# Kernel tuning notes

Measured on AMD Instinct MI355X. Metric: run time of the kernel, lower is better.

The kernel has to match this reference:

```python
import jax, jax.numpy as jnp
import numpy as np

S, B, T, A = 512, 64, 768, 512
H1 = (T + T) // 2   # 768
H2 = (T + A) // 2   # 640


def setup_inputs() -> dict:
    key = jax.random.key(0)
    ks = jax.random.split(key, 11)
    sc = 0.02
    return {
        "text": jax.random.normal(ks[0], (B, T), jnp.float32),
        "anp": jax.random.normal(ks[1], (B, A), jnp.float32),
        "text_seq": jax.random.normal(ks[2], (S, B, T), jnp.float32),
        "W11": jax.random.normal(ks[3], (2 * T, H1), jnp.float32) * sc,
        "b11": jax.random.normal(ks[4], (H1,), jnp.float32) * sc,
        "W21": jax.random.normal(ks[5], (H1, 1), jnp.float32) * sc,
        "b21": jax.random.normal(ks[6], (1,), jnp.float32) * sc,
        "W12": jax.random.normal(ks[7], (T + A, H2), jnp.float32) * sc,
        "b12": jax.random.normal(ks[8], (H2,), jnp.float32) * sc,
        "W22": jax.random.normal(ks[9], (H2, 1), jnp.float32) * sc,
        "b22": jax.random.normal(ks[10], (1,), jnp.float32) * sc,
    }


def reference(text, anp, text_seq, W11, b11, W21, b21, W12, b12, W22, b22):
    t = text_seq.shape[-1]
    # cat([text_seq[i], text]) @ W11 == text_seq @ W11[:t] + text @ W11[t:]
    h1 = jnp.tanh(jnp.einsum("sbt,th->sbh", text_seq, W11[:t]) + text @ W11[t:] + b11)
    h2 = jnp.tanh(jnp.einsum("sbt,th->sbh", text_seq, W12[:t]) + anp @ W12[t:] + b12)
    s1 = h1 @ W21 + b21            # (S, B, 1)
    s2 = h2 @ W22 + b22            # (S, B, 1)
    w1 = jax.nn.softmax(s1, axis=0)
    w2 = jax.nn.softmax(s2, axis=0)
    return jnp.mean((w1 + w2) * text_seq * 0.5, axis=0)  # (B, T)
```

## Files before the change

kernel.cpp:

```cpp
#include <hip/hip_runtime.h>
#include <stdint.h>

#define S_DIM 512
#define B_DIM 64
#define T_DIM 768
#define A_DIM 512
#define H1_DIM 768
#define H2_DIM 640
#define N_DIM (H1_DIM + H2_DIM)
#define M_DIM (S_DIM * B_DIM)
#define K_DIM T_DIM
#define NSLOT 22

typedef short s16x8 __attribute__((ext_vector_type(8)));
typedef float f32x4 __attribute__((ext_vector_type(4)));

__device__ __forceinline__ unsigned short f2bf(float f) {
    unsigned u = __float_as_uint(f);
    u += 0x7fffu + ((u >> 16) & 1u);
    return (unsigned short)(u >> 16);
}

#define BIAS_BLKS  (22 * 8)
#define ZOUT_BLKS  12
#define CONVW_BLKS (22 * 12)
#define CONVA_BLKS (M_DIM * K_DIM / 4 / 1024)
#define PREP_BLKS  (BIAS_BLKS + ZOUT_BLKS + CONVW_BLKS + CONVA_BLKS)

__global__ __launch_bounds__(256) void prep_kernel(const float* __restrict__ ts,
                                                   const float* __restrict__ text,
                                                   const float* __restrict__ anp,
                                                   const float* __restrict__ W11,
                                                   const float* __restrict__ b11,
                                                   const float* __restrict__ W12,
                                                   const float* __restrict__ b12,
                                                   unsigned short* __restrict__ Abf,
                                                   unsigned short* __restrict__ Bt,
                                                   float* __restrict__ cbias,
                                                   float* __restrict__ out) {
    const int blk = blockIdx.x;
    __shared__ float lds[64 * 65];
    if (blk < BIAS_BLKS) {
        const int c = blk >> 3;
        const int g = blk & 7;
        const int w = threadIdx.x >> 6;
        const int l = threadIdx.x & 63;
        float acc[8] = {0.f, 0.f, 0.f, 0.f, 0.f, 0.f, 0.f, 0.f};
        int n;
        if (c < 12) {
            n = c * 64 + l;
            const float* wcol = W11 + (size_t)T_DIM * H1_DIM + n;
            const int k0 = w * 192;
            #pragma unroll 4
            for (int k = k0; k < k0 + 192; ++k) {
                float wv = wcol[(size_t)k * H1_DIM];
                #pragma unroll
                for (int i = 0; i < 8; ++i)
                    acc[i] = fmaf(text[(g * 8 + i) * T_DIM + k], wv, acc[i]);
            }
        } else {
            n = H1_DIM + (c - 12) * 64 + l;
            const float* wcol = W12 + (size_t)T_DIM * H2_DIM + (n - H1_DIM);
            const int k0 = w * 128;
            #pragma unroll 4
            for (int k = k0; k < k0 + 128; ++k) {
                float wv = wcol[(size_t)k * H2_DIM];
                #pragma unroll
                for (int i = 0; i < 8; ++i)
                    acc[i] = fmaf(anp[(g * 8 + i) * A_DIM + k], wv, acc[i]);
            }
        }
        #pragma unroll
        for (int i = 0; i < 8; ++i) red_store: lds[w * 512 + i * 64 + l] = acc[i];
        __syncthreads();
        const int i2 = threadIdx.x >> 6;
        const float base = (c < 12) ? b11[n] : b12[n - H1_DIM];
        #pragma unroll
        for (int rep = 0; rep < 2; ++rep) {
            const int i = i2 + rep * 4;
            float s = (lds[i * 64 + l] + lds[512 + i * 64 + l]) +
                      (lds[1024 + i * 64 + l] + lds[1536 + i * 64 + l]);
            cbias[(g * 8 + i) * N_DIM + n] = base + s;
        }
    } else if (blk < BIAS_BLKS + ZOUT_BLKS) {
        const int i0 = (blk - BIAS_BLKS) * 1024 + threadIdx.x;
        float4 z = {0.f, 0.f, 0.f, 0.f};
        float4* o4 = (float4*)out;
        o4[i0] = z; o4[i0 + 256] = z; o4[i0 + 512] = z; o4[i0 + 768] = z;
    } else if (blk < BIAS_BLKS + ZOUT_BLKS + CONVW_BLKS) {
        const int t  = blk - BIAS_BLKS - ZOUT_BLKS;
        const int nt = t / 12, kt = t % 12;
        const int n0 = nt * 64, k0 = kt * 64;
        const int lo = threadIdx.x & 63;
        const int hi = threadIdx.x >> 6;
        const float* Wp;  int ld;
        if (nt < 12) { Wp = W11 + n0;            ld = H1_DIM; }
        else         { Wp = W12 + (n0 - H1_DIM); ld = H2_DIM; }
        #pragma unroll
        for (int r = 0; r < 16; ++r) {
            int kl = hi * 16 + r;
            lds[kl * 65 + lo] = Wp[(size_t)(k0 + kl) * ld + lo];
        }
        __syncthreads();
        #pragma unroll
        for (int r = 0; r < 16; ++r) {
            int nl = hi * 16 + r;
            Bt[(size_t)(n0 + nl) * K_DIM + k0 + lo] = f2bf(lds[lo * 65 + nl]);
        }
    } else {
        int i0 = (blk - BIAS_BLKS - ZOUT_BLKS - CONVW_BLKS) * 1024 + threadIdx.x;
        float4 v0 = ((const float4*)ts)[i0];
        float4 v1 = ((const float4*)ts)[i0 + 256];
        float4 v2 = ((const float4*)ts)[i0 + 512];
        float4 v3 = ((const float4*)ts)[i0 + 768];
        ushort4 o0, o1, o2, o3;
        o0.x = f2bf(v0.x); o0.y = f2bf(v0.y); o0.z = f2bf(v0.z); o0.w = f2bf(v0.w);
        o1.x = f2bf(v1.x); o1.y = f2bf(v1.y); o1.z = f2bf(v1.z); o1.w = f2bf(v1.w);
        o2.x = f2bf(v2.x); o2.y = f2bf(v2.y); o2.z = f2bf(v2.z); o2.w = f2bf(v2.w);
        o3.x = f2bf(v3.x); o3.y = f2bf(v3.y); o3.z = f2bf(v3.z); o3.w = f2bf(v3.w);
        ((ushort4*)Abf)[i0]       = o0;
        ((ushort4*)Abf)[i0 + 256] = o1;
        ((ushort4*)Abf)[i0 + 512] = o2;
        ((ushort4*)Abf)[i0 + 768] = o3;
    }
}

#define BM 128
#define BN 128
#define BK 64

__global__ __launch_bounds__(256, 3) void gemm_score_kernel(
        const unsigned short* __restrict__ A,
        const unsigned short* __restrict__ Bt,
        const float* __restrict__ cbias,
        const float* __restrict__ W21,
        const float* __restrict__ W22,
        float* __restrict__ part) {
    __shared__ __align__(16) unsigned short As[BM * BK];
    __shared__ __align__(16) unsigned short Bs[BN * BK];
    const int tid  = threadIdx.x;
    const int lb   = blockIdx.x;
    const int xcd  = lb & 7;
    const int ib   = lb >> 3;
    const int m0   = ((ib / 11) * 8 + xcd) * BM;
    const int n0   = (ib % 11) * BN;
    const int lane = tid & 63;
    const int wave = tid >> 6;
    const int wm   = wave & 1;
    const int wn   = wave >> 1;
    const int quad = lane >> 4;
    const int col  = lane & 15;
    const int cswz = col & 7;

    f32x4 acc[4][4] = {};

    const int wrow = lane >> 3;
    const int kof  = (((lane & 7) ^ wrow) & 7) * 8;

    for (int k0 = 0; k0 < K_DIM; k0 += BK) {
        #pragma unroll
        for (int p = 0; p < 4; ++p) {
            const int r0 = p * 32 + wave * 8;
            __builtin_amdgcn_global_load_lds(
                (__attribute__((address_space(1))) void*)&A[(size_t)(m0 + r0 + wrow) * K_DIM + k0 + kof],
                (__attribute__((address_space(3))) void*)&As[r0 * BK],
                16, 0, 0);
            __builtin_amdgcn_global_load_lds(
                (__attribute__((address_space(1))) void*)&Bt[(size_t)(n0 + r0 + wrow) * K_DIM + k0 + kof],
                (__attribute__((address_space(3))) void*)&Bs[r0 * BK],
                16, 0, 0);
        }
        __syncthreads();
        #pragma unroll
        for (int kk = 0; kk < BK; kk += 32) {
            s16x8 af[4], bf[4];
            const int ch = ((kk >> 3) + quad) ^ cswz;
            #pragma unroll
            for (int i = 0; i < 4; ++i)
                af[i] = *(const s16x8*)&As[(wm * 64 + i * 16 + col) * BK + ch * 8];
            #pragma unroll
            for (int j = 0; j < 4; ++j)
                bf[j] = *(const s16x8*)&Bs[(wn * 64 + j * 16 + col) * BK + ch * 8];
            #pragma unroll
            for (int i = 0; i < 4; ++i)
                #pragma unroll
                for (int j = 0; j < 4; ++j)
                    acc[i][j] = __builtin_amdgcn_mfma_f32_16x16x32_bf16(af[i], bf[j], acc[i][j], 0, 0, 0);
        }
        __syncthreads();
    }

    const int half = (n0 >= H1_DIM) ? 1 : 0;
    const int jb   = n0 >> 7;
    const float* w2p = half ? (W22 - H1_DIM) : W21;
    int   ncol[4];
    float w2v[4];
    #pragma unroll
    for (int j = 0; j < 4; ++j) {
        ncol[j] = n0 + wn * 64 + j * 16 + col;
        w2v[j]  = w2p[ncol[j]];
    }
    float* pc = part + (jb * 2 + wn) * M_DIM;
    #pragma unroll
    for (int i = 0; i < 4; ++i) {
        #pragma unroll
        for (int r = 0; r < 4; ++r) {
            int row_local = wm * 64 + i * 16 + quad * 4 + r;
            int b = row_local & (B_DIM - 1);
            int s = (m0 + row_local) >> 6;
            float v = 0.f;
            #pragma unroll
            for (int j = 0; j < 4; ++j) {
                float pre = acc[i][j][r] + cbias[b * N_DIM + ncol[j]];
                float ex  = __expf(2.f * pre);
                float th  = 1.f - 2.f * __builtin_amdgcn_rcpf(ex + 1.f);
                v = fmaf(th, w2v[j], v);
            }
            v += __shfl_xor(v, 1);
            v += __shfl_xor(v, 2);
            v += __shfl_xor(v, 4);
            v += __shfl_xor(v, 8);
            if (col == 0) pc[b * S_DIM + s] = v;
        }
    }
}

__global__ __launch_bounds__(512) void softmax_kernel(const float* __restrict__ part,
                                                      float* __restrict__ wsum) {
    const int b = blockIdx.x, s = threadIdx.x;
    __shared__ float redm[16], reds[16];
    float v0 = 0.f, v1 = 0.f;
    #pragma unroll
    for (int sl = 0; sl < 12; ++sl)       v0 += part[sl * M_DIM + b * S_DIM + s];
    #pragma unroll
    for (int sl = 12; sl < NSLOT; ++sl)   v1 += part[sl * M_DIM + b * S_DIM + s];
    float m0 = v0, m1 = v1;
    #pragma unroll
    for (int off = 32; off > 0; off >>= 1) {
        m0 = fmaxf(m0, __shfl_xor(m0, off));
        m1 = fmaxf(m1, __shfl_xor(m1, off));
    }
    const int w = s >> 6;
    if ((s & 63) == 0) { redm[w] = m0; redm[8 + w] = m1; }
    __syncthreads();
    m0 = redm[0]; m1 = redm[8];
    #pragma unroll
    for (int i = 1; i < 8; ++i) { m0 = fmaxf(m0, redm[i]); m1 = fmaxf(m1, redm[8 + i]); }
    float e0 = expf(v0 - m0), e1 = expf(v1 - m1);
    float s0 = e0, s1 = e1;
    #pragma unroll
    for (int off = 32; off > 0; off >>= 1) {
        s0 += __shfl_xor(s0, off);
        s1 += __shfl_xor(s1, off);
    }
    if ((s & 63) == 0) { reds[w] = s0; reds[8 + w] = s1; }
    __syncthreads();
    s0 = reds[0]; s1 = reds[8];
    #pragma unroll
    for (int i = 1; i < 8; ++i) { s0 += reds[i]; s1 += reds[8 + i]; }
    wsum[b * S_DIM + s] = e0 / s0 + e1 / s1;
}

__global__ __launch_bounds__(128) void wmean_kernel(const unsigned short* __restrict__ Abf,
                                                    const float* __restrict__ wsum,
                                                    float* __restrict__ out) {
    const int b  = blockIdx.x;
    const int tp = blockIdx.y * 128 + threadIdx.x;
    const int s0 = blockIdx.z * 128;
    const unsigned short* base = Abf + (size_t)b * T_DIM + tp * 2;
    const float* wp = wsum + b * S_DIM;
    float a0 = 0.f, a1 = 0.f, c0 = 0.f, c1 = 0.f;
    #pragma unroll 4
    for (int s = s0; s < s0 + 128; s += 2) {
        float w0 = wp[s], w1 = wp[s + 1];
        unsigned u0 = *(const unsigned*)(base + (size_t)s * (B_DIM * T_DIM));
        unsigned u1 = *(const unsigned*)(base + (size_t)(s + 1) * (B_DIM * T_DIM));
        a0 = fmaf(w0, __uint_as_float(u0 << 16),          a0);
        a1 = fmaf(w0, __uint_as_float(u0 & 0xffff0000u),  a1);
        c0 = fmaf(w1, __uint_as_float(u1 << 16),          c0);
        c1 = fmaf(w1, __uint_as_float(u1 & 0xffff0000u),  c1);
    }
    atomicAdd(&out[b * T_DIM + tp * 2],     (a0 + c0) * (0.5f / (float)S_DIM));
    atomicAdd(&out[b * T_DIM + tp * 2 + 1], (a1 + c1) * (0.5f / (float)S_DIM));
}

extern "C" void kernel_launch(void* const* d_in, const int* in_sizes, int n_in,
                              void* d_out, int out_size, void* d_ws, size_t ws_size,
                              hipStream_t stream) {
    const float* text = (const float*)d_in[0];
    const float* anp  = (const float*)d_in[1];
    const float* ts   = (const float*)d_in[2];
    const float* W11  = (const float*)d_in[3];
    const float* b11  = (const float*)d_in[4];
    const float* W21  = (const float*)d_in[5];
    const float* W12  = (const float*)d_in[7];
    const float* b12  = (const float*)d_in[8];
    const float* W22  = (const float*)d_in[9];
    float* out = (float*)d_out;

    char* ws = (char*)d_ws;
    unsigned short* Abf = (unsigned short*)ws;
    unsigned short* Bt  = (unsigned short*)(ws + 50331648);
    float* cbias = (float*)(ws + 50331648 + 2162688);
    float* part  = (float*)(ws + 50331648 + 2162688 + 360448);
    float* wsum  = (float*)(ws + 50331648 + 2162688 + 360448 + 2883584);

    prep_kernel<<<PREP_BLKS, 256, 0, stream>>>(
        ts, text, anp, W11, b11, W12, b12, Abf, Bt, cbias, out);
    gemm_score_kernel<<<(M_DIM / BM) * (N_DIM / BN), 256, 0, stream>>>(
        Abf, Bt, cbias, W21, W22, part);
    softmax_kernel<<<B_DIM, 512, 0, stream>>>(part, wsum);
    wmean_kernel<<<dim3(B_DIM, 3, 4), 128, 0, stream>>>(Abf, wsum, out);
}
```

Baseline: 298.3 us.

## Fuse bf16 conversion of activations into GEMM loads and merge softmax with weighted mean

The separate pass that converts text_seq to a bf16 copy is removed. The GEMM now reads fp32 text_seq through registers, packs it to bf16 and writes it to swizzled LDS itself. The softmax and weighted-mean kernels are merged: each block recomputes the softmax for its batch row, then reduces fp32 text_seq over S in LDS. This drops the output zeroing and the atomics. It saves writing and rereading the 50 MB bf16 copy, but the GEMM A-tile load is now synchronous through registers instead of global_load_lds, and the mean pass reads fp32 with the softmax recomputed 12 times per batch row.

```diff
diff --git a/kernel.cpp b/kernel.cpp
--- a/kernel.cpp
+++ b/kernel.cpp
@@ -21,23 +21,22 @@
     return (unsigned short)(u >> 16);
 }
 
+__device__ __forceinline__ unsigned pk2(float a, float b) {
+    return (unsigned)f2bf(a) | ((unsigned)f2bf(b) << 16);
+}
+
 #define BIAS_BLKS  (22 * 8)
-#define ZOUT_BLKS  12
 #define CONVW_BLKS (22 * 12)
-#define CONVA_BLKS (M_DIM * K_DIM / 4 / 1024)
-#define PREP_BLKS  (BIAS_BLKS + ZOUT_BLKS + CONVW_BLKS + CONVA_BLKS)
-
-__global__ __launch_bounds__(256) void prep_kernel(const float* __restrict__ ts,
-                                                   const float* __restrict__ text,
+#define PREP_BLKS  (BIAS_BLKS + CONVW_BLKS)
+
+__global__ __launch_bounds__(256) void prep_kernel(const float* __restrict__ text,
                                                    const float* __restrict__ anp,
                                                    const float* __restrict__ W11,
                                                    const float* __restrict__ b11,
                                                    const float* __restrict__ W12,
                                                    const float* __restrict__ b12,
-                                                   unsigned short* __restrict__ Abf,
                                                    unsigned short* __restrict__ Bt,
-                                                   float* __restrict__ cbias,
-                                                   float* __restrict__ out) {
+                                                   float* __restrict__ cbias) {
     const int blk = blockIdx.x;
     __shared__ float lds[64 * 65];
     if (blk < BIAS_BLKS) {
@@ -71,7 +70,7 @@
             }
         }
         #pragma unroll
-        for (int i = 0; i < 8; ++i) red_store: lds[w * 512 + i * 64 + l] = acc[i];
+        for (int i = 0; i < 8; ++i) lds[w * 512 + i * 64 + l] = acc[i];
         __syncthreads();
         const int i2 = threadIdx.x >> 6;
         const float base = (c < 12) ? b11[n] : b12[n - H1_DIM];
@@ -82,13 +81,8 @@
                       (lds[1024 + i * 64 + l] + lds[1536 + i * 64 + l]);
             cbias[(g * 8 + i) * N_DIM + n] = base + s;
         }
-    } else if (blk < BIAS_BLKS + ZOUT_BLKS) {
-        const int i0 = (blk - BIAS_BLKS) * 1024 + threadIdx.x;
-        float4 z = {0.f, 0.f, 0.f, 0.f};
-        float4* o4 = (float4*)out;
-        o4[i0] = z; o4[i0 + 256] = z; o4[i0 + 512] = z; o4[i0 + 768] = z;
-    } else if (blk < BIAS_BLKS + ZOUT_BLKS + CONVW_BLKS) {
-        const int t  = blk - BIAS_BLKS - ZOUT_BLKS;
+    } else {
+        const int t  = blk - BIAS_BLKS;
         const int nt = t / 12, kt = t % 12;
         const int n0 = nt * 64, k0 = kt * 64;
         const int lo = threadIdx.x & 63;
@@ -107,21 +101,6 @@
             int nl = hi * 16 + r;
             Bt[(size_t)(n0 + nl) * K_DIM + k0 + lo] = f2bf(lds[lo * 65 + nl]);
         }
-    } else {
-        int i0 = (blk - BIAS_BLKS - ZOUT_BLKS - CONVW_BLKS) * 1024 + threadIdx.x;
-        float4 v0 = ((const float4*)ts)[i0];
-        float4 v1 = ((const float4*)ts)[i0 + 256];
-        float4 v2 = ((const float4*)ts)[i0 + 512];
-        float4 v3 = ((const float4*)ts)[i0 + 768];
-        ushort4 o0, o1, o2, o3;
-        o0.x = f2bf(v0.x); o0.y = f2bf(v0.y); o0.z = f2bf(v0.z); o0.w = f2bf(v0.w);
-        o1.x = f2bf(v1.x); o1.y = f2bf(v1.y); o1.z = f2bf(v1.z); o1.w = f2bf(v1.w);
-        o2.x = f2bf(v2.x); o2.y = f2bf(v2.y); o2.z = f2bf(v2.z); o2.w = f2bf(v2.w);
-        o3.x = f2bf(v3.x); o3.y = f2bf(v3.y); o3.z = f2bf(v3.z); o3.w = f2bf(v3.w);
-        ((ushort4*)Abf)[i0]       = o0;
-        ((ushort4*)Abf)[i0 + 256] = o1;
-        ((ushort4*)Abf)[i0 + 512] = o2;
-        ((ushort4*)Abf)[i0 + 768] = o3;
     }
 }
 
@@ -130,7 +109,7 @@
 #define BK 64
 
 __global__ __launch_bounds__(256, 3) void gemm_score_kernel(
-        const unsigned short* __restrict__ A,
+        const float* __restrict__ ts,
         const unsigned short* __restrict__ Bt,
         const float* __restrict__ cbias,
         const float* __restrict__ W21,
@@ -158,17 +137,34 @@
     const int kof  = (((lane & 7) ^ wrow) & 7) * 8;
 
     for (int k0 = 0; k0 < K_DIM; k0 += BK) {
+        float4 av[4][2];
+        #pragma unroll
+        for (int j = 0; j < 4; ++j) {
+            const int c = tid + 256 * j;
+            const float4* src = (const float4*)(
+                ts + (size_t)(m0 + (c >> 3)) * K_DIM + k0 + (c & 7) * 8);
+            av[j][0] = src[0];
+            av[j][1] = src[1];
+        }
         #pragma unroll
         for (int p = 0; p < 4; ++p) {
             const int r0 = p * 32 + wave * 8;
-            __builtin_amdgcn_global_load_lds(
-                (__attribute__((address_space(1))) void*)&A[(size_t)(m0 + r0 + wrow) * K_DIM + k0 + kof],
-                (__attribute__((address_space(3))) void*)&As[r0 * BK],
-                16, 0, 0);
             __builtin_amdgcn_global_load_lds(
                 (__attribute__((address_space(1))) void*)&Bt[(size_t)(n0 + r0 + wrow) * K_DIM + k0 + kof],
                 (__attribute__((address_space(3))) void*)&Bs[r0 * BK],
                 16, 0, 0);
+        }
+        #pragma unroll
+        for (int j = 0; j < 4; ++j) {
+            const int c   = tid + 256 * j;
+            const int row = c >> 3;
+            const int cs  = (c & 7) ^ (row & 7);
+            uint4 q;
+            q.x = pk2(av[j][0].x, av[j][0].y);
+            q.y = pk2(av[j][0].z, av[j][0].w);
+            q.z = pk2(av[j][1].x, av[j][1].y);
+            q.w = pk2(av[j][1].z, av[j][1].w);
+            *(uint4*)&As[row * BK + cs * 8] = q;
         }
         __syncthreads();
         #pragma unroll
@@ -225,10 +221,15 @@
     }
 }
 
-__global__ __launch_bounds__(512) void softmax_kernel(const float* __restrict__ part,
-                                                      float* __restrict__ wsum) {
-    const int b = blockIdx.x, s = threadIdx.x;
+__global__ __launch_bounds__(512) void smwm_kernel(const float* __restrict__ part,
+                                                   const float* __restrict__ ts,
+                                                   float* __restrict__ out) {
+    const int b  = blockIdx.x;
+    const int tc = blockIdx.y;
+    __shared__ float wlds[512];
     __shared__ float redm[16], reds[16];
+    __shared__ float acc2[1024];
+    const int s = threadIdx.x;
     float v0 = 0.f, v1 = 0.f;
     #pragma unroll
     for (int sl = 0; sl < 12; ++sl)       v0 += part[sl * M_DIM + b * S_DIM + s];
@@ -258,30 +259,30 @@
     s0 = reds[0]; s1 = reds[8];
     #pragma unroll
     for (int i = 1; i < 8; ++i) { s0 += reds[i]; s1 += reds[8 + i]; }
-    wsum[b * S_DIM + s] = e0 / s0 + e1 / s1;
-}
-
-__global__ __launch_bounds__(128) void wmean_kernel(const unsigned short* __restrict__ Abf,
-                                                    const float* __restrict__ wsum,
-                                                    float* __restrict__ out) {
-    const int b  = blockIdx.x;
-    const int tp = blockIdx.y * 128 + threadIdx.x;
-    const int s0 = blockIdx.z * 128;
-    const unsigned short* base = Abf + (size_t)b * T_DIM + tp * 2;
-    const float* wp = wsum + b * S_DIM;
-    float a0 = 0.f, a1 = 0.f, c0 = 0.f, c1 = 0.f;
+    wlds[s] = e0 / s0 + e1 / s1;
+    __syncthreads();
+
+    const int tpl = threadIdx.x & 31;
+    const int ss  = threadIdx.x >> 5;
+    const float* base = ts + (size_t)b * T_DIM + (tc * 32 + tpl) * 2;
+    float a0 = 0.f, a1 = 0.f;
     #pragma unroll 4
-    for (int s = s0; s < s0 + 128; s += 2) {
-        float w0 = wp[s], w1 = wp[s + 1];
-        unsigned u0 = *(const unsigned*)(base + (size_t)s * (B_DIM * T_DIM));
-        unsigned u1 = *(const unsigned*)(base + (size_t)(s + 1) * (B_DIM * T_DIM));
-        a0 = fmaf(w0, __uint_as_float(u0 << 16),          a0);
-        a1 = fmaf(w0, __uint_as_float(u0 & 0xffff0000u),  a1);
-        c0 = fmaf(w1, __uint_as_float(u1 << 16),          c0);
-        c1 = fmaf(w1, __uint_as_float(u1 & 0xffff0000u),  c1);
-    }
-    atomicAdd(&out[b * T_DIM + tp * 2],     (a0 + c0) * (0.5f / (float)S_DIM));
-    atomicAdd(&out[b * T_DIM + tp * 2 + 1], (a1 + c1) * (0.5f / (float)S_DIM));
+    for (int i = 0; i < 32; ++i) {
+        const int sv = ss + i * 16;
+        const float2 u = *(const float2*)(base + (size_t)sv * (B_DIM * T_DIM));
+        const float wv = wlds[sv];
+        a0 = fmaf(wv, u.x, a0);
+        a1 = fmaf(wv, u.y, a1);
+    }
+    acc2[ss * 64 + tpl * 2]     = a0;
+    acc2[ss * 64 + tpl * 2 + 1] = a1;
+    __syncthreads();
+    if (threadIdx.x < 64) {
+        float sum = 0.f;
+        #pragma unroll
+        for (int k = 0; k < 16; ++k) sum += acc2[k * 64 + threadIdx.x];
+        out[b * T_DIM + tc * 64 + threadIdx.x] = sum * (0.5f / (float)S_DIM);
+    }
 }
 
 extern "C" void kernel_launch(void* const* d_in, const int* in_sizes, int n_in,
@@ -299,16 +300,13 @@
     float* out = (float*)d_out;
 
     char* ws = (char*)d_ws;
-    unsigned short* Abf = (unsigned short*)ws;
-    unsigned short* Bt  = (unsigned short*)(ws + 50331648);
-    float* cbias = (float*)(ws + 50331648 + 2162688);
-    float* part  = (float*)(ws + 50331648 + 2162688 + 360448);
-    float* wsum  = (float*)(ws + 50331648 + 2162688 + 360448 + 2883584);
+    unsigned short* Bt  = (unsigned short*)ws;
+    float* cbias = (float*)(ws + 2162688);
+    float* part  = (float*)(ws + 2162688 + 360448);
 
     prep_kernel<<<PREP_BLKS, 256, 0, stream>>>(
-        ts, text, anp, W11, b11, W12, b12, Abf, Bt, cbias, out);
+        text, anp, W11, b11, W12, b12, Bt, cbias);
     gemm_score_kernel<<<(M_DIM / BM) * (N_DIM / BN), 256, 0, stream>>>(
-        Abf, Bt, cbias, W21, W22, part);
-    softmax_kernel<<<B_DIM, 512, 0, stream>>>(part, wsum);
-    wmean_kernel<<<dim3(B_DIM, 3, 4), 128, 0, stream>>>(Abf, wsum, out);
-}
+        ts, Bt, cbias, W21, W22, part);
+    smwm_kernel<<<dim3(B_DIM, 12), 512, 0, stream>>>(part, ts, out);
+}
```

After: 325.1 us. 9.0% more time.

## Fuse softmax into weighted-mean kernel and drop output zeroing and atomics

Applied to the files above, without the earlier changes.

Merges the softmax and weighted-mean kernels into a single kernel gridded over batch and 64-column chunks. Each block recomputes the softmax weights for its batch row into LDS, then reduces over the sequence with 16 sequence-slices per block and sums the partials in shared memory. Because each output element now has one writer, the zeroing blocks in prep and the atomicAdds are removed. In exchange the softmax is recomputed 12 times per batch row, which repeats the reads of the partial-score buffer.

```diff
diff --git a/kernel.cpp b/kernel.cpp
--- a/kernel.cpp
+++ b/kernel.cpp
@@ -22,10 +22,9 @@
 }
 
 #define BIAS_BLKS  (22 * 8)
-#define ZOUT_BLKS  12
 #define CONVW_BLKS (22 * 12)
 #define CONVA_BLKS (M_DIM * K_DIM / 4 / 1024)
-#define PREP_BLKS  (BIAS_BLKS + ZOUT_BLKS + CONVW_BLKS + CONVA_BLKS)
+#define PREP_BLKS  (BIAS_BLKS + CONVW_BLKS + CONVA_BLKS)
 
 __global__ __launch_bounds__(256) void prep_kernel(const float* __restrict__ ts,
                                                    const float* __restrict__ text,
@@ -36,8 +35,7 @@
                                                    const float* __restrict__ b12,
                                                    unsigned short* __restrict__ Abf,
                                                    unsigned short* __restrict__ Bt,
-                                                   float* __restrict__ cbias,
-                                                   float* __restrict__ out) {
+                                                   float* __restrict__ cbias) {
     const int blk = blockIdx.x;
     __shared__ float lds[64 * 65];
     if (blk < BIAS_BLKS) {
@@ -71,7 +69,7 @@
             }
         }
         #pragma unroll
-        for (int i = 0; i < 8; ++i) red_store: lds[w * 512 + i * 64 + l] = acc[i];
+        for (int i = 0; i < 8; ++i) lds[w * 512 + i * 64 + l] = acc[i];
         __syncthreads();
         const int i2 = threadIdx.x >> 6;
         const float base = (c < 12) ? b11[n] : b12[n - H1_DIM];
@@ -82,13 +80,8 @@
                       (lds[1024 + i * 64 + l] + lds[1536 + i * 64 + l]);
             cbias[(g * 8 + i) * N_DIM + n] = base + s;
         }
-    } else if (blk < BIAS_BLKS + ZOUT_BLKS) {
-        const int i0 = (blk - BIAS_BLKS) * 1024 + threadIdx.x;
-        float4 z = {0.f, 0.f, 0.f, 0.f};
-        float4* o4 = (float4*)out;
-        o4[i0] = z; o4[i0 + 256] = z; o4[i0 + 512] = z; o4[i0 + 768] = z;
-    } else if (blk < BIAS_BLKS + ZOUT_BLKS + CONVW_BLKS) {
-        const int t  = blk - BIAS_BLKS - ZOUT_BLKS;
+    } else if (blk < BIAS_BLKS + CONVW_BLKS) {
+        const int t  = blk - BIAS_BLKS;
         const int nt = t / 12, kt = t % 12;
         const int n0 = nt * 64, k0 = kt * 64;
         const int lo = threadIdx.x & 63;
@@ -108,7 +101,7 @@
             Bt[(size_t)(n0 + nl) * K_DIM + k0 + lo] = f2bf(lds[lo * 65 + nl]);
         }
     } else {
-        int i0 = (blk - BIAS_BLKS - ZOUT_BLKS - CONVW_BLKS) * 1024 + threadIdx.x;
+        int i0 = (blk - BIAS_BLKS - CONVW_BLKS) * 1024 + threadIdx.x;
         float4 v0 = ((const float4*)ts)[i0];
         float4 v1 = ((const float4*)ts)[i0 + 256];
         float4 v2 = ((const float4*)ts)[i0 + 512];
@@ -225,10 +218,15 @@
     }
 }
 
-__global__ __launch_bounds__(512) void softmax_kernel(const float* __restrict__ part,
-                                                      float* __restrict__ wsum) {
-    const int b = blockIdx.x, s = threadIdx.x;
+__global__ __launch_bounds__(512) void smwm_kernel(const float* __restrict__ part,
+                                                   const unsigned short* __restrict__ Abf,
+                                                   float* __restrict__ out) {
+    const int b  = blockIdx.x;
+    const int tc = blockIdx.y;
+    __shared__ float wlds[512];
     __shared__ float redm[16], reds[16];
+    __shared__ float acc2[1024];
+    const int s = threadIdx.x;
     float v0 = 0.f, v1 = 0.f;
     #pragma unroll
     for (int sl = 0; sl < 12; ++sl)       v0 += part[sl * M_DIM + b * S_DIM + s];
@@ -258,30 +256,30 @@
     s0 = reds[0]; s1 = reds[8];
     #pragma unroll
     for (int i = 1; i < 8; ++i) { s0 += reds[i]; s1 += reds[8 + i]; }
-    wsum[b * S_DIM + s] = e0 / s0 + e1 / s1;
-}
-
-__global__ __launch_bounds__(128) void wmean_kernel(const unsigned short* __restrict__ Abf,
-                                                    const float* __restrict__ wsum,
-                                                    float* __restrict__ out) {
-    const int b  = blockIdx.x;
-    const int tp = blockIdx.y * 128 + threadIdx.x;
-    const int s0 = blockIdx.z * 128;
-    const unsigned short* base = Abf + (size_t)b * T_DIM + tp * 2;
-    const float* wp = wsum + b * S_DIM;
-    float a0 = 0.f, a1 = 0.f, c0 = 0.f, c1 = 0.f;
+    wlds[s] = e0 / s0 + e1 / s1;
+    __syncthreads();
+
+    const int tpl = threadIdx.x & 31;
+    const int ss  = threadIdx.x >> 5;
+    const unsigned short* base = Abf + (size_t)b * T_DIM + (tc * 32 + tpl) * 2;
+    float a0 = 0.f, a1 = 0.f;
     #pragma unroll 4
-    for (int s = s0; s < s0 + 128; s += 2) {
-        float w0 = wp[s], w1 = wp[s + 1];
-        unsigned u0 = *(const unsigned*)(base + (size_t)s * (B_DIM * T_DIM));
-        unsigned u1 = *(const unsigned*)(base + (size_t)(s + 1) * (B_DIM * T_DIM));
-        a0 = fmaf(w0, __uint_as_float(u0 << 16),          a0);
-        a1 = fmaf(w0, __uint_as_float(u0 & 0xffff0000u),  a1);
-        c0 = fmaf(w1, __uint_as_float(u1 << 16),          c0);
-        c1 = fmaf(w1, __uint_as_float(u1 & 0xffff0000u),  c1);
-    }
-    atomicAdd(&out[b * T_DIM + tp * 2],     (a0 + c0) * (0.5f / (float)S_DIM));
-    atomicAdd(&out[b * T_DIM + tp * 2 + 1], (a1 + c1) * (0.5f / (float)S_DIM));
+    for (int i = 0; i < 32; ++i) {
+        const int sv = ss + i * 16;
+        const unsigned u = *(const unsigned*)(base + (size_t)sv * (B_DIM * T_DIM));
+        const float wv = wlds[sv];
+        a0 = fmaf(wv, __uint_as_float(u << 16),         a0);
+        a1 = fmaf(wv, __uint_as_float(u & 0xffff0000u), a1);
+    }
+    acc2[ss * 64 + tpl * 2]     = a0;
+    acc2[ss * 64 + tpl * 2 + 1] = a1;
+    __syncthreads();
+    if (threadIdx.x < 64) {
+        float sum = 0.f;
+        #pragma unroll
+        for (int k = 0; k < 16; ++k) sum += acc2[k * 64 + threadIdx.x];
+        out[b * T_DIM + tc * 64 + threadIdx.x] = sum * (0.5f / (float)S_DIM);
+    }
 }
 
 extern "C" void kernel_launch(void* const* d_in, const int* in_sizes, int n_in,
@@ -303,12 +301,10 @@
     unsigned short* Bt  = (unsigned short*)(ws + 50331648);
     float* cbias = (float*)(ws + 50331648 + 2162688);
     float* part  = (float*)(ws + 50331648 + 2162688 + 360448);
-    float* wsum  = (float*)(ws + 50331648 + 2162688 + 360448 + 2883584);
 
     prep_kernel<<<PREP_BLKS, 256, 0, stream>>>(
-        ts, text, anp, W11, b11, W12, b12, Abf, Bt, cbias, out);
+        ts, text, anp, W11, b11, W12, b12, Abf, Bt, cbias);
     gemm_score_kernel<<<(M_DIM / BM) * (N_DIM / BN), 256, 0, stream>>>(
         Abf, Bt, cbias, W21, W22, part);
-    softmax_kernel<<<B_DIM, 512, 0, stream>>>(part, wsum);
-    wmean_kernel<<<dim3(B_DIM, 3, 4), 128, 0, stream>>>(Abf, wsum, out);
-}
+    smwm_kernel<<<dim3(B_DIM, 12), 512, 0, stream>>>(part, Abf, out);
+}
```

After: 296.5 us. No clear change (-0.6%).
